# Kernel tuning notes

Measured on AMD Instinct MI355X. Metric: run time of the kernel, lower is better.

Reference implementation:

```python
import jax, jax.numpy as jnp
import numpy as np

H = 128  # hidden_dim


def _lstm_dir(x, w_ih, w_hh, b, reverse):
    """Single-direction LSTM over x:[B,T,I]. PyTorch gate order (i,f,g,o)."""
    B = x.shape[0]
    gx = jnp.einsum('bti,gi->btg', x, w_ih) + b        # [B,T,4H] input-side gates, one batched GEMM
    gx = jnp.swapaxes(gx, 0, 1)                        # [T,B,4H]
    if reverse:
        gx = gx[::-1]

    def step(carry, g_x):
        h, c = carry
        g = g_x + h @ w_hh.T                           # [B,4H]
        i, f, gg, o = jnp.split(g, 4, axis=-1)
        i = jax.nn.sigmoid(i)
        f = jax.nn.sigmoid(f)
        gg = jnp.tanh(gg)
        o = jax.nn.sigmoid(o)
        c = f * c + i * gg
        h = o * jnp.tanh(c)
        return (h, c), h

    init = (jnp.zeros((B, H), x.dtype), jnp.zeros((B, H), x.dtype))
    (hT, cT), hs = jax.lax.scan(step, init, gx)        # hs:[T,B,H]
    hs = jnp.swapaxes(hs, 0, 1)                        # [B,T,H]
    if reverse:
        hs = hs[:, ::-1]
    return hs, hT, cT


def _bilstm_layer(x, pf, pb):
    hf, hTf, cTf = _lstm_dir(x, *pf, reverse=False)
    hb, hTb, cTb = _lstm_dir(x, *pb, reverse=True)
    return jnp.concatenate([hf, hb], axis=-1), (hTf, cTf), (hTb, cTb)


def setup_inputs() -> dict:
    key = jax.random.key(0)
    ks = jax.random.split(key, 13)
    s = 1.0 / np.sqrt(H)
    B, T, I = 256, 512, 24
    d = {"x": jax.random.normal(ks[0], (B, T, I), jnp.float32)}
    # layer 0 input dim = 24; layer 1 input dim = 2*H = 256
    dims = {"l0f": I, "l0b": I, "l1f": 2 * H, "l1b": 2 * H}
    i = 1
    for tag, din in dims.items():
        d[f"w_ih_{tag}"] = jax.random.uniform(ks[i], (4 * H, din), jnp.float32, -s, s); i += 1
        d[f"w_hh_{tag}"] = jax.random.uniform(ks[i], (4 * H, H), jnp.float32, -s, s); i += 1
        d[f"b_{tag}"] = jax.random.uniform(ks[i], (4 * H,), jnp.float32, -s, s); i += 1
    return d


def reference(x,
              w_ih_l0f, w_hh_l0f, b_l0f, w_ih_l0b, w_hh_l0b, b_l0b,
              w_ih_l1f, w_hh_l1f, b_l1f, w_ih_l1b, w_hh_l1b, b_l1b):
    # Layer 0 (bidirectional)
    y0, (hTf0, cTf0), (hTb0, cTb0) = _bilstm_layer(
        x, (w_ih_l0f, w_hh_l0f, b_l0f), (w_ih_l0b, w_hh_l0b, b_l0b))
    # Inter-layer dropout is identity in eval mode.
    # Layer 1 (bidirectional)
    y1, (hTf1, cTf1), (hTb1, cTb1) = _bilstm_layer(
        y0, (w_ih_l1f, w_hh_l1f, b_l1f), (w_ih_l1b, w_hh_l1b, b_l1b))
    # PyTorch h_n/c_n layout: [num_layers*num_dirs, B, H] ordered l0f,l0b,l1f,l1b
    h_n = jnp.stack([hTf0, hTb0, hTf1, hTb1], axis=0)
    c_n = jnp.stack([cTf0, cTb0, cTf1, cTb1], axis=0)
    return y1, h_n, c_n
```

## Files before the change

kernel.cpp:

```cpp
#include <hip/hip_runtime.h>
#include <hip/hip_bf16.h>
#include <stdint.h>

#define Bn 256
#define Tn 512
#define Hn 128
#define G4 512
#define Mn (Bn*Tn)

typedef __attribute__((ext_vector_type(8))) short s16x8;
typedef __attribute__((ext_vector_type(4))) float f32x4;

__device__ __forceinline__ float b2f(unsigned short u) {
    union { unsigned int i; float f; } v; v.i = ((unsigned int)u) << 16; return v.f;
}
__device__ __forceinline__ unsigned short f2b(float f) {
    union { float f; unsigned int i; } v; v.f = f;
    unsigned int x = v.i;
    unsigned int r = (x + 0x7FFFu + ((x >> 16) & 1u)) >> 16;
    return (unsigned short)r;
}
__device__ __forceinline__ unsigned int pk2(float a, float b) {
    __hip_bfloat162 t = __float22bfloat162_rn(make_float2(a, b));
    union { __hip_bfloat162 v; unsigned int u; } c; c.v = t; return c.u;
}
__device__ __forceinline__ s16x8 cvt8v(const float* p) {
    f32x4 a = *(const f32x4*)p;
    f32x4 b = *(const f32x4*)(p + 4);
    s16x8 r;
    r[0] = (short)f2b(a[0]); r[1] = (short)f2b(a[1]);
    r[2] = (short)f2b(a[2]); r[3] = (short)f2b(a[3]);
    r[4] = (short)f2b(b[0]); r[5] = (short)f2b(b[1]);
    r[6] = (short)f2b(b[2]); r[7] = (short)f2b(b[3]);
    return r;
}
__device__ __forceinline__ float sigm(float x) {
    return __builtin_amdgcn_rcpf(1.f + __expf(-x));
}
__device__ __forceinline__ float tanh_f(float x) {
    return 1.f - 2.f * __builtin_amdgcn_rcpf(1.f + __expf(2.f * x));
}
__device__ __forceinline__ void gload16(const void* gsrc, void* lds) {
    __builtin_amdgcn_global_load_lds(
        (const __attribute__((address_space(1))) unsigned int*)gsrc,
        (__attribute__((address_space(3))) unsigned int*)lds, 16, 0, 0);
}
__device__ __forceinline__ void ldsbar() {
    asm volatile("s_waitcnt lgkmcnt(0)\n\ts_barrier" ::: "memory");
}

__global__ __launch_bounds__(256)
void prep(const float* __restrict__ x,
          const float* __restrict__ w0f, const float* __restrict__ w0b,
          const float* __restrict__ w1f, const float* __restrict__ w1b,
          unsigned short* __restrict__ xb,
          unsigned short* __restrict__ w0bf,
          unsigned short* __restrict__ w1bf)
{
    int tid = blockIdx.x * 256 + threadIdx.x;
    int nthr = gridDim.x * 256;
    for (int idx = tid; idx < Mn * 32; idx += nthr) {
        int row = idx >> 5, col = idx & 31;
        xb[idx] = f2b(col < 24 ? x[row * 24 + col] : 0.f);
    }
    for (int idx = tid; idx < 2 * 512 * 32; idx += nthr) {
        int d = idx >> 14, rem = idx & 16383;
        int n = rem >> 5, col = rem & 31;
        const float* w = d ? w0b : w0f;
        w0bf[idx] = f2b(col < 24 ? w[n * 24 + col] : 0.f);
    }
    for (int idx = tid; idx < 2 * 512 * 256; idx += nthr) {
        int d = idx >> 17, rem = idx & 131071;
        const float* w = d ? w1b : w1f;
        w1bf[idx] = f2b(w[rem]);
    }
}

template<int BK, int KOUT>
__global__ __launch_bounds__(256, 2)
void gemm_tile(const unsigned short* __restrict__ A, int lda,
               const unsigned short* __restrict__ W,
               unsigned short* __restrict__ gx)
{
    constexpr int GR = BK / 8;
    constexpr int SWM = (GR >= 8) ? 7 : (GR - 1);
    constexpr int ASZ = 128 * BK * 2;
    constexpr int GOFF = (BK == 128) ? 0 : 2 * ASZ;
    constexpr int SMEM = 2 * ASZ + ((BK == 128) ? 0 : 4 * 16 * 68 * 4);
    __shared__ char smem[SMEM];
    unsigned short* Atile = (unsigned short*)smem;
    unsigned short* Btile = (unsigned short*)(smem + ASZ);

    const int K = BK * KOUT;
    const int mb = blockIdx.x;
    const int nb = blockIdx.y;
    const int dir = nb >> 2, ncol0 = (nb & 3) * 128;
    const int row0 = mb * 128;
    const unsigned short* Asrc = A + (size_t)row0 * lda;
    const unsigned short* Bsrc = W + (size_t)dir * 512 * K + (size_t)ncol0 * K;
    unsigned short* out = gx + (size_t)dir * Mn * G4;

    const int tid = threadIdx.x;
    const int w = tid >> 6, l = tid & 63;
    const int q = l >> 4, i = l & 15;
    const int wm = w >> 1, wn = w & 1;

    f32x4 acc[4][4];
#pragma unroll
    for (int a = 0; a < 4; ++a)
#pragma unroll
        for (int b = 0; b < 4; ++b) acc[a][b] = f32x4{0.f, 0.f, 0.f, 0.f};

    for (int ko = 0; ko < KOUT; ++ko) {
#pragma unroll
        for (int it = 0; it < (128 * GR) / 256; ++it) {
            int g = it * 256 + tid;
            int row = g / GR, p = g % GR;
            int gi = p ^ (row & SWM);
            gload16(Asrc + (size_t)row * lda + ko * BK + gi * 8,
                    (char*)Atile + g * 16);
        }
#pragma unroll
        for (int it = 0; it < (128 * GR) / 256; ++it) {
            int g = it * 256 + tid;
            int row = g / GR, p = g % GR;
            int gi = p ^ (row & SWM);
            gload16(Bsrc + (size_t)row * K + ko * BK + gi * 8,
                    (char*)Btile + g * 16);
        }
        __syncthreads();
#pragma unroll
        for (int kf = 0; kf < BK / 32; ++kf) {
            s16x8 af[4], bf[4];
#pragma unroll
            for (int mt = 0; mt < 4; ++mt) {
                int ar = wm * 64 + mt * 16 + i;
                int p = (kf * 4 + q) ^ (ar & SWM);
                af[mt] = *(const s16x8*)((char*)Atile + (ar * GR + p) * 16);
            }
#pragma unroll
            for (int nt = 0; nt < 4; ++nt) {
                int br = wn * 64 + nt * 16 + i;
                int p = (kf * 4 + q) ^ (br & SWM);
                bf[nt] = *(const s16x8*)((char*)Btile + (br * GR + p) * 16);
            }
#pragma unroll
            for (int mt = 0; mt < 4; ++mt)
#pragma unroll
                for (int nt = 0; nt < 4; ++nt)
                    acc[mt][nt] = __builtin_amdgcn_mfma_f32_16x16x32_bf16(
                        af[mt], bf[nt], acc[mt][nt], 0, 0, 0);
        }
        __syncthreads();
    }

    float* gbufw = (float*)(smem + GOFF) + w * (16 * 68);
#pragma unroll
    for (int mt = 0; mt < 4; ++mt) {
#pragma unroll
        for (int nt = 0; nt < 4; ++nt)
#pragma unroll
            for (int r = 0; r < 4; ++r)
                gbufw[(q * 4 + r) * 68 + nt * 16 + i] = acc[mt][nt][r];
        __syncthreads();
#pragma unroll
        for (int it2 = 0; it2 < 2; ++it2) {
            int rr = (l >> 3) + it2 * 8;
            int cc = (l & 7) * 8;
            const float* gsrc = gbufw + rr * 68 + cc;
            uint4 pv;
            pv.x = pk2(gsrc[0], gsrc[1]);
            pv.y = pk2(gsrc[2], gsrc[3]);
            pv.z = pk2(gsrc[4], gsrc[5]);
            pv.w = pk2(gsrc[6], gsrc[7]);
            *(uint4*)(out + (size_t)(row0 + wm * 64 + mt * 16 + rr) * G4
                          + ncol0 + wn * 64 + cc) = pv;
        }
        __syncthreads();
    }
}

template<int LAYER>
__global__ __launch_bounds__(256, 1)
void lstm_rec(const unsigned short* __restrict__ gx,
              const float* __restrict__ Whf,
              const float* __restrict__ Whb,
              const float* __restrict__ biasf,
              const float* __restrict__ biasb,
              float* __restrict__ y,
              unsigned short* __restrict__ y0b,
              float* __restrict__ hn,
              float* __restrict__ cn)
{
    const int b0  = blockIdx.x * 2;
    const int dir = blockIdx.y;
    const float* Wh   = dir ? Whb : Whf;
    const float* bias = dir ? biasb : biasf;
    const unsigned short* gxd = gx + (size_t)dir * Mn * G4;

    const int tid = threadIdx.x;
    const int w = tid >> 6, l = tid & 63;
    const int q = l >> 4, i = l & 15;

    __shared__ unsigned short hbuf[16][136];
    __shared__ float Gs[2][512];

    for (int idx = tid; idx < 16 * 136; idx += 256)
        ((unsigned short*)hbuf)[idx] = 0;

    s16x8 wh[8][4];
#pragma unroll
    for (int nt = 0; nt < 8; ++nt) {
        int n = w * 128 + nt * 16 + i;
#pragma unroll
        for (int kf = 0; kf < 4; ++kf)
            wh[nt][kf] = cvt8v(Wh + (size_t)n * Hn + kf * 32 + q * 8);
    }

    const int m = tid >> 7;
    const int j = tid & 127;
    const int b = b0 + m;
    const float bi = bias[j],       bfv = bias[128 + j];
    const float bg = bias[256 + j], bo  = bias[384 + j];
    float c = 0.f, hlast = 0.f;

    const s16x8* ah0p = (const s16x8*)&hbuf[i][0 * 32 + q * 8];
    const s16x8* ah1p = (const s16x8*)&hbuf[i][1 * 32 + q * 8];
    const s16x8* ah2p = (const s16x8*)&hbuf[i][2 * 32 + q * 8];
    const s16x8* ah3p = (const s16x8*)&hbuf[i][3 * 32 + q * 8];
    float* gw0 = &Gs[0][w * 128 + i];
    float* gw1 = &Gs[1][w * 128 + i];
    const float* gr = &Gs[m][j];
    unsigned short* hw = &hbuf[m][j];

    const intptr_t gstep = dir ? -(intptr_t)G4 : (intptr_t)G4;
    const unsigned short* p0 =
        gxd + ((size_t)b * Tn + (dir ? Tn - 1 : 0)) * G4 + j;
    const unsigned short* gp_pre = p0 + 8 * gstep;
    const intptr_t ystep = dir ? (intptr_t)-256 : (intptr_t)256;
    float* yp = y + ((size_t)b * Tn + (dir ? Tn - 1 : 0)) * 256 + dir * 128 + j;
    unsigned short* y0p =
        y0b + ((size_t)b * Tn + (dir ? Tn - 1 : 0)) * 256 + dir * 128 + j;

    unsigned short bufA[4][8], bufB[4][8];
#pragma unroll
    for (int f = 0; f < 8; ++f) {
        const unsigned short* gp = p0 + f * gstep;
        bufA[0][f] = gp[0];
        bufA[1][f] = gp[128];
        bufA[2][f] = gp[256];
        bufA[3][f] = gp[384];
    }

    __syncthreads();

    auto do8 = [&](unsigned short (&useB)[4][8], unsigned short (&ldB)[4][8],
                   int sb) {
#pragma unroll
        for (int f = 0; f < 8; ++f) {
            const int s = sb + f;

            s16x8 ah0 = *ah0p, ah1 = *ah1p, ah2 = *ah2p, ah3 = *ah3p;

            ldB[0][f] = gp_pre[0];
            ldB[1][f] = gp_pre[128];
            ldB[2][f] = gp_pre[256];
            ldB[3][f] = gp_pre[384];
            if (s < Tn - 9) gp_pre += gstep;

            f32x4 acc[8];
#pragma unroll
            for (int nt = 0; nt < 8; ++nt) acc[nt] = f32x4{0.f, 0.f, 0.f, 0.f};
#pragma unroll
            for (int nt = 0; nt < 8; ++nt)
                acc[nt] = __builtin_amdgcn_mfma_f32_16x16x32_bf16(
                    ah0, wh[nt][0], acc[nt], 0, 0, 0);
#pragma unroll
            for (int nt = 0; nt < 8; ++nt)
                acc[nt] = __builtin_amdgcn_mfma_f32_16x16x32_bf16(
                    ah1, wh[nt][1], acc[nt], 0, 0, 0);
#pragma unroll
            for (int nt = 0; nt < 8; ++nt)
                acc[nt] = __builtin_amdgcn_mfma_f32_16x16x32_bf16(
                    ah2, wh[nt][2], acc[nt], 0, 0, 0);
#pragma unroll
            for (int nt = 0; nt < 8; ++nt)
                acc[nt] = __builtin_amdgcn_mfma_f32_16x16x32_bf16(
                    ah3, wh[nt][3], acc[nt], 0, 0, 0);

            const float pi = b2f(useB[0][f]) + bi;
            const float pf = b2f(useB[1][f]) + bfv;
            const float pg = b2f(useB[2][f]) + bg;
            const float po = b2f(useB[3][f]) + bo;

            if (q == 0) {
#pragma unroll
                for (int nt = 0; nt < 8; ++nt) {
                    gw0[nt * 16] = acc[nt][0];
                    gw1[nt * 16] = acc[nt][1];
                }
            }
            ldsbar();

            float g_i = gr[0]   + pi;
            float g_f = gr[128] + pf;
            float g_g = gr[256] + pg;
            float g_o = gr[384] + po;
            float iv = sigm(g_i), fv = sigm(g_f), ov = sigm(g_o);
            float gv = tanh_f(g_g);
            c = fv * c + iv * gv;
            float h = ov * tanh_f(c);
            hlast = h;
            unsigned int hp;
            asm("v_cvt_pk_bf16_f32 %0, %1, %2" : "=v"(hp) : "v"(h), "v"(h));
            unsigned short hb = (unsigned short)hp;
            *hw = hb;
            if (LAYER == 0) *y0p = hb;
            else            *yp  = h;
            yp += ystep; y0p += ystep;

            ldsbar();
        }
    };

    for (int sb = 0; sb < Tn; sb += 16) {
        do8(bufA, bufB, sb);
        do8(bufB, bufA, sb + 8);
    }

    const int slot = LAYER * 2 + dir;
    hn[((size_t)slot * Bn + b) * Hn + j] = hlast;
    cn[((size_t)slot * Bn + b) * Hn + j] = c;
}

extern "C" void kernel_launch(void* const* d_in, const int* in_sizes, int n_in,
                              void* d_out, int out_size, void* d_ws, size_t ws_size,
                              hipStream_t stream)
{
    const float* x     = (const float*)d_in[0];
    const float* wih0f = (const float*)d_in[1];
    const float* whh0f = (const float*)d_in[2];
    const float* b0f   = (const float*)d_in[3];
    const float* wih0b = (const float*)d_in[4];
    const float* whh0b = (const float*)d_in[5];
    const float* b0b   = (const float*)d_in[6];
    const float* wih1f = (const float*)d_in[7];
    const float* whh1f = (const float*)d_in[8];
    const float* b1f   = (const float*)d_in[9];
    const float* wih1b = (const float*)d_in[10];
    const float* whh1b = (const float*)d_in[11];
    const float* b1b   = (const float*)d_in[12];

    float* y  = (float*)d_out;
    float* hn = y + (size_t)Mn * 256;
    float* cn = hn + (size_t)4 * Bn * Hn;
    unsigned short* gx = (unsigned short*)d_ws;

    unsigned short* scr  = (unsigned short*)d_out;
    unsigned short* y0b  = scr;
    unsigned short* xb   = scr + (size_t)Mn * 256;
    unsigned short* w0bf = xb  + (size_t)Mn * 32;
    unsigned short* w1bf = w0bf + 2 * 512 * 32;

    prep<<<2048, 256, 0, stream>>>(x, wih0f, wih0b, wih1f, wih1b, xb, w0bf, w1bf);

    dim3 gg(1024, 8), gb(256);
    dim3 rg(128, 2), rb(256);

    gemm_tile<32, 1><<<gg, gb, 0, stream>>>(xb, 32, w0bf, gx);
    lstm_rec<0><<<rg, rb, 0, stream>>>(gx, whh0f, whh0b, b0f, b0b, y, y0b, hn, cn);
    gemm_tile<128, 2><<<gg, gb, 0, stream>>>(y0b, 256, w1bf, gx);
    lstm_rec<1><<<rg, rb, 0, stream>>>(gx, whh1f, whh1b, b1f, b1b, y, y0b, hn, cn);
}
```

Before: 994.7 us.

## Compute all four gates per wave to skip the LDS gate exchange

Each wave's weight tiles are reassigned so it computes the i, f, g and o gate pre-activations for its own 32 hidden units. A lane's recurrent gate sums can then be taken straight from its MFMA accumulators. This removes the shared-memory gate buffer, its stores and loads, and one workgroup barrier per timestep. The MFMA count stays the same, but the lane-to-hidden-unit mapping and the hidden-state LDS layout change, which adds correctness risk in the indexing.

```diff
diff --git a/kernel.cpp b/kernel.cpp
--- a/kernel.cpp
+++ b/kernel.cpp
@@ -199,39 +199,39 @@
     const unsigned short* gxd = gx + (size_t)dir * Mn * G4;
 
     const int tid = threadIdx.x;
-    const int w = tid >> 6, l = tid & 63;
+    const int w = tid >> 6;
+    const int l = tid & 63;
     const int q = l >> 4, i = l & 15;
-
-    __shared__ unsigned short hbuf[16][136];
-    __shared__ float Gs[2][512];
-
-    for (int idx = tid; idx < 16 * 136; idx += 256)
+    const int u = q & 1;
+    const int r = q >> 1;
+    const int j = 32 * w + 16 * u + i;
+    const int b = b0 + r;
+
+    __shared__ __align__(16) unsigned short hbuf[2][160];
+
+    for (int idx = tid; idx < 2 * 160; idx += 256)
         ((unsigned short*)hbuf)[idx] = 0;
 
-    s16x8 wh[8][4];
-#pragma unroll
-    for (int nt = 0; nt < 8; ++nt) {
-        int n = w * 128 + nt * 16 + i;
-#pragma unroll
-        for (int kf = 0; kf < 4; ++kf)
-            wh[nt][kf] = cvt8v(Wh + (size_t)n * Hn + kf * 32 + q * 8);
-    }
-
-    const int m = tid >> 7;
-    const int j = tid & 127;
-    const int b = b0 + m;
+    s16x8 wh[4][2][4];
+#pragma unroll
+    for (int g = 0; g < 4; ++g)
+#pragma unroll
+        for (int ut = 0; ut < 2; ++ut) {
+            int n = 128 * g + 32 * w + 16 * ut + i;
+#pragma unroll
+            for (int kf = 0; kf < 4; ++kf)
+                wh[g][ut][kf] = cvt8v(Wh + (size_t)n * Hn + kf * 32 + q * 8);
+        }
+
     const float bi = bias[j],       bfv = bias[128 + j];
     const float bg = bias[256 + j], bo  = bias[384 + j];
     float c = 0.f, hlast = 0.f;
 
-    const s16x8* ah0p = (const s16x8*)&hbuf[i][0 * 32 + q * 8];
-    const s16x8* ah1p = (const s16x8*)&hbuf[i][1 * 32 + q * 8];
-    const s16x8* ah2p = (const s16x8*)&hbuf[i][2 * 32 + q * 8];
-    const s16x8* ah3p = (const s16x8*)&hbuf[i][3 * 32 + q * 8];
-    float* gw0 = &Gs[0][w * 128 + i];
-    float* gw1 = &Gs[1][w * 128 + i];
-    const float* gr = &Gs[m][j];
-    unsigned short* hw = &hbuf[m][j];
+    const s16x8* ah0p = (const s16x8*)&hbuf[i >> 3][0 * 32 + q * 8];
+    const s16x8* ah1p = (const s16x8*)&hbuf[i >> 3][1 * 32 + q * 8];
+    const s16x8* ah2p = (const s16x8*)&hbuf[i >> 3][2 * 32 + q * 8];
+    const s16x8* ah3p = (const s16x8*)&hbuf[i >> 3][3 * 32 + q * 8];
+    unsigned short* hw = &hbuf[r][j];
 
     const intptr_t gstep = dir ? -(intptr_t)G4 : (intptr_t)G4;
     const unsigned short* p0 =
@@ -267,45 +267,51 @@
             ldB[2][f] = gp_pre[256];
             ldB[3][f] = gp_pre[384];
             if (s < Tn - 9) gp_pre += gstep;
-
-            f32x4 acc[8];
-#pragma unroll
-            for (int nt = 0; nt < 8; ++nt) acc[nt] = f32x4{0.f, 0.f, 0.f, 0.f};
-#pragma unroll
-            for (int nt = 0; nt < 8; ++nt)
-                acc[nt] = __builtin_amdgcn_mfma_f32_16x16x32_bf16(
-                    ah0, wh[nt][0], acc[nt], 0, 0, 0);
-#pragma unroll
-            for (int nt = 0; nt < 8; ++nt)
-                acc[nt] = __builtin_amdgcn_mfma_f32_16x16x32_bf16(
-                    ah1, wh[nt][1], acc[nt], 0, 0, 0);
-#pragma unroll
-            for (int nt = 0; nt < 8; ++nt)
-                acc[nt] = __builtin_amdgcn_mfma_f32_16x16x32_bf16(
-                    ah2, wh[nt][2], acc[nt], 0, 0, 0);
-#pragma unroll
-            for (int nt = 0; nt < 8; ++nt)
-                acc[nt] = __builtin_amdgcn_mfma_f32_16x16x32_bf16(
-                    ah3, wh[nt][3], acc[nt], 0, 0, 0);
-
             const float pi = b2f(useB[0][f]) + bi;
             const float pf = b2f(useB[1][f]) + bfv;
             const float pg = b2f(useB[2][f]) + bg;
             const float po = b2f(useB[3][f]) + bo;
 
-            if (q == 0) {
-#pragma unroll
-                for (int nt = 0; nt < 8; ++nt) {
-                    gw0[nt * 16] = acc[nt][0];
-                    gw1[nt * 16] = acc[nt][1];
-                }
-            }
-            ldsbar();
-
-            float g_i = gr[0]   + pi;
-            float g_f = gr[128] + pf;
-            float g_g = gr[256] + pg;
-            float g_o = gr[384] + po;
+            f32x4 acc[4][2];
+#pragma unroll
+            for (int g = 0; g < 4; ++g)
+#pragma unroll
+                for (int ut = 0; ut < 2; ++ut)
+                    acc[g][ut] = f32x4{0.f, 0.f, 0.f, 0.f};
+#pragma unroll
+            for (int g = 0; g < 4; ++g)
+#pragma unroll
+                for (int ut = 0; ut < 2; ++ut)
+                    acc[g][ut] = __builtin_amdgcn_mfma_f32_16x16x32_bf16(
+                        ah0, wh[g][ut][0], acc[g][ut], 0, 0, 0);
+#pragma unroll
+            for (int g = 0; g < 4; ++g)
+#pragma unroll
+                for (int ut = 0; ut < 2; ++ut)
+                    acc[g][ut] = __builtin_amdgcn_mfma_f32_16x16x32_bf16(
+                        ah1, wh[g][ut][1], acc[g][ut], 0, 0, 0);
+#pragma unroll
+            for (int g = 0; g < 4; ++g)
+#pragma unroll
+                for (int ut = 0; ut < 2; ++ut)
+                    acc[g][ut] = __builtin_amdgcn_mfma_f32_16x16x32_bf16(
+                        ah2, wh[g][ut][2], acc[g][ut], 0, 0, 0);
+#pragma unroll
+            for (int g = 0; g < 4; ++g)
+#pragma unroll
+                for (int ut = 0; ut < 2; ++ut)
+                    acc[g][ut] = __builtin_amdgcn_mfma_f32_16x16x32_bf16(
+                        ah3, wh[g][ut][3], acc[g][ut], 0, 0, 0);
+
+            const float s_i = u ? acc[0][1][0] : acc[0][0][0];
+            const float s_f = u ? acc[1][1][0] : acc[1][0][0];
+            const float s_g = u ? acc[2][1][0] : acc[2][0][0];
+            const float s_o = u ? acc[3][1][0] : acc[3][0][0];
+
+            float g_i = s_i + pi;
+            float g_f = s_f + pf;
+            float g_g = s_g + pg;
+            float g_o = s_o + po;
             float iv = sigm(g_i), fv = sigm(g_f), ov = sigm(g_o);
             float gv = tanh_f(g_g);
             c = fv * c + iv * gv;
```

Result: no change. 1.005 ms (+1.1%).
